# Performance work log

Hardware: AMD Instinct MI355X
Metric: run time of the kernel (lower is better)

## Reference

```python
import jax, jax.numpy as jnp
import numpy as np

HIDDEN_DIM = 2048
HEAD_NUM = 16
HEAD_DIM = HIDDEN_DIM // HEAD_NUM


def setup_inputs() -> dict:
    key = jax.random.key(0)
    ks = jax.random.split(key, 9)
    B, S, H = 2, 2048, HIDDEN_DIM
    scale = 1.0 / np.sqrt(H)
    X = jax.random.normal(ks[0], (B, S, H), dtype=jnp.float32)
    Wq = jax.random.normal(ks[1], (H, H), dtype=jnp.float32) * scale
    bq = jnp.zeros((H,), dtype=jnp.float32)
    Wk = jax.random.normal(ks[2], (H, H), dtype=jnp.float32) * scale
    bk = jnp.zeros((H,), dtype=jnp.float32)
    Wv = jax.random.normal(ks[3], (H, H), dtype=jnp.float32) * scale
    bv = jnp.zeros((H,), dtype=jnp.float32)
    Wo = jax.random.normal(ks[4], (H, H), dtype=jnp.float32) * scale
    bo = jnp.zeros((H,), dtype=jnp.float32)
    return {"X": X, "Wq": Wq, "bq": bq, "Wk": Wk, "bk": bk,
            "Wv": Wv, "bv": bv, "Wo": Wo, "bo": bo}


def reference(X, Wq, bq, Wk, bk, Wv, bv, Wo, bo):
    B, S, H = X.shape
    # QKV projections (nn.Linear applies x @ W.T + b; weights here stored as [in, out])
    Q = X @ Wq + bq
    K = X @ Wk + bk
    V = X @ Wv + bv
    # [B, heads, S, head_dim]
    q = Q.reshape(B, S, HEAD_NUM, HEAD_DIM).transpose(0, 2, 1, 3)
    k = K.reshape(B, S, HEAD_NUM, HEAD_DIM).transpose(0, 2, 1, 3)
    v = V.reshape(B, S, HEAD_NUM, HEAD_DIM).transpose(0, 2, 1, 3)
    scores = jnp.einsum('bhqd,bhkd->bhqk', q, k) / jnp.sqrt(jnp.float32(HEAD_DIM))
    attn = jax.nn.softmax(scores, axis=-1)  # dropout = identity in eval
    out = jnp.einsum('bhqk,bhkd->bhqd', attn, v)
    out = out.transpose(0, 2, 1, 3).reshape(B, S, H)
    return out @ Wo + bo
```

## Files before the change

### kernel.cpp

```cpp
#include <hip/hip_runtime.h>
#include <hip/hip_bf16.h>
#include <stdint.h>


#define Bc 2
#define Sc 2048
#define Hc 2048
#define NHc 16
#define Dc 128
#define Mc 4096

typedef unsigned short ushortT;
typedef float f32x4 __attribute__((ext_vector_type(4)));
typedef _Float16 f16x8 __attribute__((ext_vector_type(8)));

#define MFMAH(a, b, c) __builtin_amdgcn_mfma_f32_16x16x32_f16((a), (b), (c), 0, 0, 0)

static __device__ __forceinline__ ushortT f2h(float x) {
    _Float16 h = (_Float16)x;
    return __builtin_bit_cast(unsigned short, h);
}

static __device__ __forceinline__ void load_lds16(const ushortT* g, ushortT* l) {
    __builtin_amdgcn_global_load_lds(
        (__attribute__((address_space(1))) void*)(g),
        (__attribute__((address_space(3))) void*)(l), 16, 0, 0);
}

__global__ __launch_bounds__(256) void pack_a(
    const float* __restrict__ src, ushortT* __restrict__ dst)
{
    const int mt = blockIdx.x, kt = blockIdx.y;
    const int t = threadIdx.x;
    const int kq = t & 15;
    const int r0 = t >> 4;
    ushortT* tile = dst + ((size_t)(mt * 32 + kt)) * 8192;
#pragma unroll
    for (int rr = 0; rr < 8; ++rr) {
        const int row = r0 + rr * 16;
        const float4 v = *(const float4*)(src + (size_t)(mt * 128 + row) * Hc + kt * 64 + kq * 4);
        _Float16 h[4] = {(_Float16)v.x, (_Float16)v.y, (_Float16)v.z, (_Float16)v.w};
        const int gid = kq >> 1, halfg = kq & 1;
        const int gp = gid ^ (row & 7);
        *(uint2*)(tile + (size_t)row * 64 + gp * 8 + halfg * 4) = *(uint2*)h;
    }
}

__global__ __launch_bounds__(256) void pack_b(
    const float* __restrict__ W0, const float* __restrict__ W1,
    const float* __restrict__ W2, const float* __restrict__ W3,
    ushortT* __restrict__ dst)
{
    const int nt = blockIdx.x, kt = blockIdx.y, which = blockIdx.z;
    const float* W = (which == 0) ? W0 : (which == 1) ? W1 : (which == 2) ? W2 : W3;
    const int t = threadIdx.x;
    const int n = t & 127;
    const int g0 = (t >> 7) * 4;
    ushortT* tile = dst + (size_t)which * 4194304 + ((size_t)(nt * 32 + kt)) * 8192;
#pragma unroll
    for (int gi = 0; gi < 4; ++gi) {
        const int g = g0 + gi;
        _Float16 h[8];
#pragma unroll
        for (int j = 0; j < 8; ++j)
            h[j] = (_Float16)W[(size_t)(kt * 64 + g * 8 + j) * Hc + nt * 128 + n];
        const int gp = g ^ (n & 7);
        *(uint4*)(tile + (size_t)n * 64 + gp * 8) = *(uint4*)h;
    }
}

#define GEMM_PROLOGUE()                                                        \
    __shared__ __align__(16) ushortT As[8192], Bs[8192];                       \
    const int tid = threadIdx.x, wv_ = tid >> 6, lane = tid & 63;              \
    const int lane16 = lane & 15, quad = lane >> 4;                            \
    const int quad4 = quad * 4;                                                \
    const int wm = (wv_ & 1) * 64, wn = (wv_ >> 1) * 64;                       \
    int aoff[4][2], boff[4][2];                                                \
    _Pragma("unroll") for (int mi = 0; mi < 4; ++mi)                           \
        _Pragma("unroll") for (int kf = 0; kf < 2; ++kf) {                     \
            const int ra = wm + mi * 16 + lane16;                              \
            aoff[mi][kf] = ra * 64 + (((kf * 4 + quad) ^ (ra & 7)) << 3);      \
            const int rb = wn + mi * 16 + lane16;                              \
            boff[mi][kf] = rb * 64 + (((kf * 4 + quad) ^ (rb & 7)) << 3);      \
        }                                                                      \
    f32x4 acc[4][4];                                                           \
    _Pragma("unroll") for (int i = 0; i < 4; ++i)                              \
        _Pragma("unroll") for (int j = 0; j < 4; ++j) {                        \
            acc[i][j][0] = 0.f; acc[i][j][1] = 0.f;                            \
            acc[i][j][2] = 0.f; acc[i][j][3] = 0.f; }                          \
    ushortT* asd = &As[wv_ * 2048];                                            \
    ushortT* bsd = &Bs[wv_ * 2048];

#define GEMM_KLOOP(at, bt)                                                     \
    for (int kt2 = 0; kt2 < 32; ++kt2) {                                       \
        _Pragma("unroll") for (int i = 0; i < 4; ++i) {                        \
            load_lds16(at + i * 512 + lane * 8, asd + i * 512);                \
            load_lds16(bt + i * 512 + lane * 8, bsd + i * 512);                \
        }                                                                      \
        at += 8192; bt += 8192;                                                \
        __syncthreads();                                                       \
        _Pragma("unroll") for (int kf = 0; kf < 2; ++kf) {                     \
            f16x8 a[4], b[4];                                                  \
            _Pragma("unroll") for (int mi = 0; mi < 4; ++mi)                   \
                a[mi] = *(const f16x8*)&As[aoff[mi][kf]];                      \
            _Pragma("unroll") for (int nj = 0; nj < 4; ++nj)                   \
                b[nj] = *(const f16x8*)&Bs[boff[nj][kf]];                      \
            _Pragma("unroll") for (int nj = 0; nj < 4; ++nj)                   \
                _Pragma("unroll") for (int mi = 0; mi < 4; ++mi)               \
                    acc[mi][nj] = MFMAH(a[mi], b[nj], acc[mi][nj]);            \
        }                                                                      \
        __syncthreads();                                                       \
    }

__global__ __launch_bounds__(256) void qkv_gemm(
    const ushortT* __restrict__ Xp, const ushortT* __restrict__ Wall,
    const float* __restrict__ bq, const float* __restrict__ bk,
    const float* __restrict__ bv,
    ushortT* __restrict__ Qd, ushortT* __restrict__ Kd, ushortT* __restrict__ Vt)
{
    const int which = blockIdx.x >> 4;
    const int nt = blockIdx.x & 15;
    const int mt = blockIdx.y;
    const ushortT* Wp = Wall + (size_t)which * 4194304;
    const float* bias = (which == 0) ? bq : (which == 1) ? bk : bv;

    GEMM_PROLOGUE();

    const ushortT* at = Xp + (size_t)(mt * 32) * 8192 + wv_ * 2048;
    const ushortT* bt = Wp + (size_t)(nt * 32) * 8192 + wv_ * 2048;
    GEMM_KLOOP(at, bt);

    const float QS = 0.08838834764831845f * 1.4426950408889634f;
#pragma unroll
    for (int nj = 0; nj < 4; ++nj) {
        const int col = nt * 128 + wn + nj * 16 + lane16;
        const float bb = bias[col];
        const int hh = col >> 7, dd = col & 127;
#pragma unroll
        for (int mi = 0; mi < 4; ++mi)
#pragma unroll
            for (int r = 0; r < 4; ++r) {
                const int m = mt * 128 + wm + mi * 16 + quad4 + r;
                const int b = m >> 11, s = m & 2047;
                float v = acc[mi][nj][r] + bb;
                if (which == 0)
                    Qd[(((size_t)(b * NHc + hh)) * Sc + s) * Dc + dd] = f2h(v * QS);
                else if (which == 1)
                    Kd[(((size_t)(b * NHc + hh)) * Sc + s) * Dc + dd] = f2h(v);
                else
                    Vt[(((size_t)(b * NHc + hh)) * Dc + dd) * Sc + s] = f2h(v);
            }
    }
}

__global__ __launch_bounds__(256) void attn(
    const ushortT* __restrict__ Qd, const ushortT* __restrict__ Kd,
    const ushortT* __restrict__ Vt, ushortT* __restrict__ AOp)
{
    const int qt = blockIdx.x, hh = blockIdx.y, bb = blockIdx.z;
    const ushortT* Qp = Qd + ((size_t)(bb * NHc + hh)) * Sc * Dc;
    const ushortT* Kp = Kd + ((size_t)(bb * NHc + hh)) * Sc * Dc;
    const ushortT* Vp = Vt + ((size_t)(bb * NHc + hh)) * Dc * Sc;

    __shared__ __align__(16) ushortT Ks[64 * 128];
    __shared__ __align__(16) ushortT Vs[128 * 64];
    __shared__ __align__(16) float   SsF[4 * 32 * 64];
    __shared__ float alphas[4 * 32], linvs[4 * 32];

    const int tid = threadIdx.x, wv_ = tid >> 6, lane = tid & 63;
    const int lane16 = lane & 15, quad = lane >> 4;
    const int quad8 = quad * 8, quad4 = quad * 4;
    const int s0 = qt * 128 + wv_ * 32;

    f16x8 q[2][4];
#pragma unroll
    for (int mi = 0; mi < 2; ++mi)
#pragma unroll
        for (int kf = 0; kf < 4; ++kf)
            q[mi][kf] = *(const f16x8*)(Qp + (size_t)(s0 + mi * 16 + lane16) * Dc + kf * 32 + quad8);

    f32x4 o[2][8];
#pragma unroll
    for (int mi = 0; mi < 2; ++mi)
#pragma unroll
        for (int dj = 0; dj < 8; ++dj) { o[mi][dj][0] = 0.f; o[mi][dj][1] = 0.f; o[mi][dj][2] = 0.f; o[mi][dj][3] = 0.f; }

    float m_run = -1e30f, l_run = 0.f;
    const int sr = lane >> 1, sch = (lane & 1) * 32;
    const int kr = tid >> 2, kseg = tid & 3;
    const int vr = tid >> 1, vseg = tid & 1;
    float* Sw = &SsF[wv_ * 2048];
    ushortT* Pw = (ushortT*)Sw;

    for (int nt = 0; nt < 32; ++nt) {
        const ushortT* ksrc = Kp + (size_t)(nt * 64 + kr) * Dc + kseg * 32;
#pragma unroll
        for (int i = 0; i < 4; ++i)
            *(uint4*)&Ks[kr * 128 + (((kseg * 4 + i) ^ (kr & 7)) << 3)] = *(const uint4*)(ksrc + i * 8);
        const ushortT* vsrc = Vp + (size_t)vr * Sc + nt * 64 + vseg * 32;
#pragma unroll
        for (int i = 0; i < 4; ++i)
            *(uint4*)&Vs[vr * 64 + (((vseg * 4 + i) ^ (vr & 7)) << 3)] = *(const uint4*)(vsrc + i * 8);
        __syncthreads();

        f32x4 sacc[2][4];
#pragma unroll
        for (int mi = 0; mi < 2; ++mi)
#pragma unroll
            for (int nj = 0; nj < 4; ++nj) { sacc[mi][nj][0] = 0.f; sacc[mi][nj][1] = 0.f; sacc[mi][nj][2] = 0.f; sacc[mi][nj][3] = 0.f; }
#pragma unroll
        for (int kf = 0; kf < 4; ++kf) {
            f16x8 kb[4];
#pragma unroll
            for (int nj = 0; nj < 4; ++nj) {
                const int row = nj * 16 + lane16;
                kb[nj] = *(const f16x8*)&Ks[row * 128 + (((kf * 4 + quad) ^ (row & 7)) << 3)];
            }
#pragma unroll
            for (int mi = 0; mi < 2; ++mi)
#pragma unroll
                for (int nj = 0; nj < 4; ++nj)
                    sacc[mi][nj] = MFMAH(q[mi][kf], kb[nj], sacc[mi][nj]);
        }
#pragma unroll
        for (int mi = 0; mi < 2; ++mi)
#pragma unroll
            for (int nj = 0; nj < 4; ++nj)
#pragma unroll
                for (int r = 0; r < 4; ++r) {
                    const int row = mi * 16 + quad4 + r, col = nj * 16 + lane16;
                    Sw[row * 64 + (((col >> 2) ^ (row & 15)) << 2) + (col & 3)] = sacc[mi][nj][r];
                }
        float svv[32];
#pragma unroll
        for (int i = 0; i < 8; ++i)
            *(float4*)&svv[i * 4] = *(const float4*)&Sw[sr * 64 + ((((sch >> 2) + i) ^ (sr & 15)) << 2)];
        float mx = svv[0];
#pragma unroll
        for (int i = 1; i < 32; ++i) mx = fmaxf(mx, svv[i]);
        mx = fmaxf(mx, __shfl_xor(mx, 1));
        const float mnew = fmaxf(m_run, mx);
        const float alpha = exp2f(m_run - mnew);
        m_run = mnew;
        float sum = 0.f;
#pragma unroll
        for (int i = 0; i < 32; ++i) { const float p = exp2f(svv[i] - mnew); svv[i] = p; sum += p; }
        sum += __shfl_xor(sum, 1);
        l_run = l_run * alpha + sum;
        if (!(lane & 1)) alphas[wv_ * 32 + sr] = alpha;
        uint32_t pu[16];
#pragma unroll
        for (int i = 0; i < 16; ++i)
            pu[i] = (uint32_t)f2h(svv[2 * i]) | ((uint32_t)f2h(svv[2 * i + 1]) << 16);
#pragma unroll
        for (int i = 0; i < 4; ++i)
            *(uint4*)&Pw[sr * 64 + ((((sch >> 3) + i) ^ (sr & 7)) << 3)] = *(uint4*)&pu[i * 4];
#pragma unroll
        for (int mi = 0; mi < 2; ++mi)
#pragma unroll
            for (int r = 0; r < 4; ++r) {
                const int row = mi * 16 + quad4 + r;
                const float av = alphas[wv_ * 32 + row];
#pragma unroll
                for (int dj = 0; dj < 8; ++dj) o[mi][dj][r] *= av;
            }
#pragma unroll
        for (int kf2 = 0; kf2 < 2; ++kf2) {
            f16x8 pa[2];
#pragma unroll
            for (int mi = 0; mi < 2; ++mi) {
                const int row = mi * 16 + lane16;
                pa[mi] = *(const f16x8*)&Pw[row * 64 + (((kf2 * 4 + quad) ^ (row & 7)) << 3)];
            }
#pragma unroll
            for (int dj = 0; dj < 8; ++dj) {
                const int row = dj * 16 + lane16;
                const f16x8 vb = *(const f16x8*)&Vs[row * 64 + (((kf2 * 4 + quad) ^ (row & 7)) << 3)];
#pragma unroll
                for (int mi = 0; mi < 2; ++mi)
                    o[mi][dj] = MFMAH(pa[mi], vb, o[mi][dj]);
            }
        }
        __syncthreads();
    }

    if (!(lane & 1)) linvs[wv_ * 32 + sr] = 1.f / l_run;
#pragma unroll
    for (int mi = 0; mi < 2; ++mi)
#pragma unroll
        for (int r = 0; r < 4; ++r) {
            const int row = mi * 16 + quad4 + r;
            const float li = linvs[wv_ * 32 + row];
            const int mrow = bb * Sc + qt * 128 + wv_ * 32 + row;
            const int mtile = mrow >> 7, rin = mrow & 127;
#pragma unroll
            for (int dj = 0; dj < 8; ++dj) {
                const int kt = hh * 2 + (dj >> 2);
                const int colin = (dj & 3) * 16 + lane16;
                const int g = colin >> 3, e = colin & 7;
                const int gp = g ^ (rin & 7);
                AOp[((size_t)(mtile * 32 + kt)) * 8192 + rin * 64 + gp * 8 + e] =
                    f2h(o[mi][dj][r] * li);
            }
        }
}

__global__ __launch_bounds__(256) void out_gemm(
    const ushortT* __restrict__ AOp, const ushortT* __restrict__ Wop,
    const float* __restrict__ bo, float* __restrict__ out)
{
    const int nt = blockIdx.x;
    const int mt = blockIdx.y;

    GEMM_PROLOGUE();

    const ushortT* at = AOp + (size_t)(mt * 32) * 8192 + wv_ * 2048;
    const ushortT* bt = Wop + (size_t)(nt * 32) * 8192 + wv_ * 2048;
    GEMM_KLOOP(at, bt);

#pragma unroll
    for (int nj = 0; nj < 4; ++nj) {
        const int col = nt * 128 + wn + nj * 16 + lane16;
        const float bb = bo[col];
#pragma unroll
        for (int mi = 0; mi < 4; ++mi)
#pragma unroll
            for (int r = 0; r < 4; ++r) {
                const int m = mt * 128 + wm + mi * 16 + quad4 + r;
                out[(size_t)m * Hc + col] = acc[mi][nj][r] + bb;
            }
    }
}

extern "C" void kernel_launch(void* const* d_in, const int* in_sizes, int n_in,
                              void* d_out, int out_size, void* d_ws, size_t ws_size,
                              hipStream_t stream) {
    (void)in_sizes; (void)n_in; (void)out_size; (void)ws_size;

    const float* X  = (const float*)d_in[0];
    const float* Wq = (const float*)d_in[1];
    const float* bq = (const float*)d_in[2];
    const float* Wk = (const float*)d_in[3];
    const float* bk = (const float*)d_in[4];
    const float* Wv = (const float*)d_in[5];
    const float* bv = (const float*)d_in[6];
    const float* Wo = (const float*)d_in[7];
    const float* bo = (const float*)d_in[8];
    float* out = (float*)d_out;

    ushortT* ws = (ushortT*)d_ws;
    const size_t E = (size_t)Mc * Hc;
    const size_t WE = (size_t)Hc * Hc;
    ushortT* Xp   = ws;
    ushortT* Wall = Xp + E;
    ushortT* Qd   = Wall + 4 * WE;
    ushortT* Kd   = Qd + E;
    ushortT* Vt   = Kd + E;
    ushortT* AOp  = Vt + E;

    pack_a<<<dim3(32, 32), 256, 0, stream>>>(X, Xp);
    pack_b<<<dim3(16, 32, 4), 256, 0, stream>>>(Wq, Wk, Wv, Wo, Wall);
    qkv_gemm<<<dim3(48, 32), 256, 0, stream>>>(Xp, Wall, bq, bk, bv, Qd, Kd, Vt);
    attn<<<dim3(16, NHc, Bc), 256, 0, stream>>>(Qd, Kd, Vt, AOp);
    out_gemm<<<dim3(16, 32), 256, 0, stream>>>(AOp, Wall + 3 * WE, bo, out);
}
```

Baseline: 523.0 us.

## Pre-tile K/V in LDS layout, use direct global-to-LDS loads, shrink softmax scratch

The QKV GEMM epilogue now writes K and V tiles already swizzled in the 64-row LDS layout, so the attention kernel can copy them with global_load_lds instead of register round trips. Softmax is processed per 16-row half using a smaller padded score buffer and separate P buffer, cutting LDS use to allow two blocks per CU (launch_bounds 256,2). V fragments are hoisted into registers once per tile. The cost is scattered epilogue stores and higher register pressure from the hoisted V fragments.

```diff
diff --git a/kernel.cpp b/kernel.cpp
--- a/kernel.cpp
+++ b/kernel.cpp
@@ -142,30 +142,39 @@
             for (int r = 0; r < 4; ++r) {
                 const int m = mt * 128 + wm + mi * 16 + quad4 + r;
                 const int b = m >> 11, s = m & 2047;
-                float v = acc[mi][nj][r] + bb;
-                if (which == 0)
-                    Qd[(((size_t)(b * NHc + hh)) * Sc + s) * Dc + dd] = f2h(v * QS);
-                else if (which == 1)
-                    Kd[(((size_t)(b * NHc + hh)) * Sc + s) * Dc + dd] = f2h(v);
-                else
-                    Vt[(((size_t)(b * NHc + hh)) * Dc + dd) * Sc + s] = f2h(v);
-            }
-    }
-}
-
-__global__ __launch_bounds__(256) void attn(
-    const ushortT* __restrict__ Qd, const ushortT* __restrict__ Kd,
+                const float v = acc[mi][nj][r] + bb;
+                const size_t bhb = (size_t)(b * NHc + hh) * (Sc * Dc);
+                if (which == 0) {
+                    Qd[bhb + (size_t)s * Dc + dd] = f2h(v * QS);
+                } else if (which == 1) {
+                    const int t2 = s >> 6, sin = s & 63;
+                    Kd[bhb + (size_t)t2 * 8192 + sin * 128 +
+                       (((dd >> 3) ^ (sin & 7)) << 3) + (dd & 7)] = f2h(v);
+                } else {
+                    const int t2 = s >> 6, sin = s & 63;
+                    Vt[bhb + (size_t)t2 * 8192 + dd * 64 +
+                       (((sin >> 3) ^ (dd & 7)) << 3) + (sin & 7)] = f2h(v);
+                }
+            }
+    }
+}
+
+#define SSTR 68
+
+__global__ __launch_bounds__(256, 2) void attn(
+    const ushortT* __restrict__ Qd, const ushortT* __restrict__ Kt,
     const ushortT* __restrict__ Vt, ushortT* __restrict__ AOp)
 {
     const int qt = blockIdx.x, hh = blockIdx.y, bb = blockIdx.z;
-    const ushortT* Qp = Qd + ((size_t)(bb * NHc + hh)) * Sc * Dc;
-    const ushortT* Kp = Kd + ((size_t)(bb * NHc + hh)) * Sc * Dc;
-    const ushortT* Vp = Vt + ((size_t)(bb * NHc + hh)) * Dc * Sc;
-
-    __shared__ __align__(16) ushortT Ks[64 * 128];
-    __shared__ __align__(16) ushortT Vs[128 * 64];
-    __shared__ __align__(16) float   SsF[4 * 32 * 64];
-    __shared__ float alphas[4 * 32], linvs[4 * 32];
+    const ushortT* Qp  = Qd + ((size_t)(bb * NHc + hh)) * Sc * Dc;
+    const ushortT* Kbh = Kt + ((size_t)(bb * NHc + hh)) * Sc * Dc;
+    const ushortT* Vbh = Vt + ((size_t)(bb * NHc + hh)) * Sc * Dc;
+
+    __shared__ __align__(16) ushortT Ks[8192];
+    __shared__ __align__(16) ushortT Vs[8192];
+    __shared__ __align__(16) float   Sbuf[4][16 * SSTR];
+    __shared__ __align__(16) ushortT Pbuf[4][1024];
+    __shared__ float alphas[4][32], linvs[4][32];
 
     const int tid = threadIdx.x, wv_ = tid >> 6, lane = tid & 63;
     const int lane16 = lane & 15, quad = lane >> 4;
@@ -185,22 +194,22 @@
 #pragma unroll
         for (int dj = 0; dj < 8; ++dj) { o[mi][dj][0] = 0.f; o[mi][dj][1] = 0.f; o[mi][dj][2] = 0.f; o[mi][dj][3] = 0.f; }
 
-    float m_run = -1e30f, l_run = 0.f;
-    const int sr = lane >> 1, sch = (lane & 1) * 32;
-    const int kr = tid >> 2, kseg = tid & 3;
-    const int vr = tid >> 1, vseg = tid & 1;
-    float* Sw = &SsF[wv_ * 2048];
-    ushortT* Pw = (ushortT*)Sw;
+    float m_run[2] = {-1e30f, -1e30f}, l_run[2] = {0.f, 0.f};
+    const int srow = lane >> 2;
+    const int scol = (lane & 3) * 16;
+    float*   Sw = Sbuf[wv_];
+    ushortT* Pw = Pbuf[wv_];
 
     for (int nt = 0; nt < 32; ++nt) {
-        const ushortT* ksrc = Kp + (size_t)(nt * 64 + kr) * Dc + kseg * 32;
-#pragma unroll
-        for (int i = 0; i < 4; ++i)
-            *(uint4*)&Ks[kr * 128 + (((kseg * 4 + i) ^ (kr & 7)) << 3)] = *(const uint4*)(ksrc + i * 8);
-        const ushortT* vsrc = Vp + (size_t)vr * Sc + nt * 64 + vseg * 32;
-#pragma unroll
-        for (int i = 0; i < 4; ++i)
-            *(uint4*)&Vs[vr * 64 + (((vseg * 4 + i) ^ (vr & 7)) << 3)] = *(const uint4*)(vsrc + i * 8);
+        const ushortT* ktile = Kbh + (size_t)nt * 8192 + wv_ * 2048;
+        const ushortT* vtile = Vbh + (size_t)nt * 8192 + wv_ * 2048;
+        ushortT* kdst = Ks + wv_ * 2048;
+        ushortT* vdst = Vs + wv_ * 2048;
+#pragma unroll
+        for (int i = 0; i < 4; ++i) {
+            load_lds16(ktile + i * 512 + lane * 8, kdst + i * 512);
+            load_lds16(vtile + i * 512 + lane * 8, vdst + i * 512);
+        }
         __syncthreads();
 
         f32x4 sacc[2][4];
@@ -222,84 +231,87 @@
                 for (int nj = 0; nj < 4; ++nj)
                     sacc[mi][nj] = MFMAH(q[mi][kf], kb[nj], sacc[mi][nj]);
         }
-#pragma unroll
-        for (int mi = 0; mi < 2; ++mi)
-#pragma unroll
-            for (int nj = 0; nj < 4; ++nj)
-#pragma unroll
-                for (int r = 0; r < 4; ++r) {
-                    const int row = mi * 16 + quad4 + r, col = nj * 16 + lane16;
-                    Sw[row * 64 + (((col >> 2) ^ (row & 15)) << 2) + (col & 3)] = sacc[mi][nj][r];
-                }
-        float svv[32];
-#pragma unroll
-        for (int i = 0; i < 8; ++i)
-            *(float4*)&svv[i * 4] = *(const float4*)&Sw[sr * 64 + ((((sch >> 2) + i) ^ (sr & 15)) << 2)];
-        float mx = svv[0];
-#pragma unroll
-        for (int i = 1; i < 32; ++i) mx = fmaxf(mx, svv[i]);
-        mx = fmaxf(mx, __shfl_xor(mx, 1));
-        const float mnew = fmaxf(m_run, mx);
-        const float alpha = exp2f(m_run - mnew);
-        m_run = mnew;
-        float sum = 0.f;
-#pragma unroll
-        for (int i = 0; i < 32; ++i) { const float p = exp2f(svv[i] - mnew); svv[i] = p; sum += p; }
-        sum += __shfl_xor(sum, 1);
-        l_run = l_run * alpha + sum;
-        if (!(lane & 1)) alphas[wv_ * 32 + sr] = alpha;
-        uint32_t pu[16];
-#pragma unroll
-        for (int i = 0; i < 16; ++i)
-            pu[i] = (uint32_t)f2h(svv[2 * i]) | ((uint32_t)f2h(svv[2 * i + 1]) << 16);
-#pragma unroll
-        for (int i = 0; i < 4; ++i)
-            *(uint4*)&Pw[sr * 64 + ((((sch >> 3) + i) ^ (sr & 7)) << 3)] = *(uint4*)&pu[i * 4];
-#pragma unroll
-        for (int mi = 0; mi < 2; ++mi)
-#pragma unroll
-            for (int r = 0; r < 4; ++r) {
-                const int row = mi * 16 + quad4 + r;
-                const float av = alphas[wv_ * 32 + row];
-#pragma unroll
-                for (int dj = 0; dj < 8; ++dj) o[mi][dj][r] *= av;
-            }
-#pragma unroll
-        for (int kf2 = 0; kf2 < 2; ++kf2) {
-            f16x8 pa[2];
-#pragma unroll
-            for (int mi = 0; mi < 2; ++mi) {
-                const int row = mi * 16 + lane16;
-                pa[mi] = *(const f16x8*)&Pw[row * 64 + (((kf2 * 4 + quad) ^ (row & 7)) << 3)];
-            }
+
+        f16x8 vb[2][8];
+#pragma unroll
+        for (int kf2 = 0; kf2 < 2; ++kf2)
 #pragma unroll
             for (int dj = 0; dj < 8; ++dj) {
                 const int row = dj * 16 + lane16;
-                const f16x8 vb = *(const f16x8*)&Vs[row * 64 + (((kf2 * 4 + quad) ^ (row & 7)) << 3)];
-#pragma unroll
-                for (int mi = 0; mi < 2; ++mi)
-                    o[mi][dj] = MFMAH(pa[mi], vb, o[mi][dj]);
+                vb[kf2][dj] = *(const f16x8*)&Vs[row * 64 + (((kf2 * 4 + quad) ^ (row & 7)) << 3)];
+            }
+
+#pragma unroll
+        for (int mi = 0; mi < 2; ++mi) {
+#pragma unroll
+            for (int nj = 0; nj < 4; ++nj)
+#pragma unroll
+                for (int r = 0; r < 4; ++r)
+                    Sw[(quad4 + r) * SSTR + nj * 16 + lane16] = sacc[mi][nj][r];
+            float sv[16];
+#pragma unroll
+            for (int i = 0; i < 4; ++i)
+                *(float4*)&sv[i * 4] = *(const float4*)&Sw[srow * SSTR + scol + i * 4];
+            float mx = sv[0];
+#pragma unroll
+            for (int i = 1; i < 16; ++i) mx = fmaxf(mx, sv[i]);
+            mx = fmaxf(mx, __shfl_xor(mx, 1));
+            mx = fmaxf(mx, __shfl_xor(mx, 2));
+            const float mnew = fmaxf(m_run[mi], mx);
+            const float alpha = exp2f(m_run[mi] - mnew);
+            m_run[mi] = mnew;
+            float sum = 0.f;
+#pragma unroll
+            for (int i = 0; i < 16; ++i) { const float p = exp2f(sv[i] - mnew); sv[i] = p; sum += p; }
+            sum += __shfl_xor(sum, 1);
+            sum += __shfl_xor(sum, 2);
+            l_run[mi] = l_run[mi] * alpha + sum;
+            if ((lane & 3) == 0) alphas[wv_][mi * 16 + srow] = alpha;
+            uint32_t pu[8];
+#pragma unroll
+            for (int i = 0; i < 8; ++i)
+                pu[i] = (uint32_t)f2h(sv[2 * i]) | ((uint32_t)f2h(sv[2 * i + 1]) << 16);
+#pragma unroll
+            for (int j = 0; j < 2; ++j) {
+                const int g = (scol >> 3) + j;
+                *(uint4*)&Pw[srow * 64 + ((g ^ (srow & 7)) << 3)] = *(uint4*)&pu[j * 4];
+            }
+#pragma unroll
+            for (int r = 0; r < 4; ++r) {
+                const float av = alphas[wv_][mi * 16 + quad4 + r];
+#pragma unroll
+                for (int dj = 0; dj < 8; ++dj) o[mi][dj][r] *= av;
+            }
+#pragma unroll
+            for (int kf2 = 0; kf2 < 2; ++kf2) {
+                const f16x8 pa = *(const f16x8*)&Pw[lane16 * 64 + (((kf2 * 4 + quad) ^ (lane16 & 7)) << 3)];
+#pragma unroll
+                for (int dj = 0; dj < 8; ++dj)
+                    o[mi][dj] = MFMAH(pa, vb[kf2][dj], o[mi][dj]);
             }
         }
         __syncthreads();
     }
 
-    if (!(lane & 1)) linvs[wv_ * 32 + sr] = 1.f / l_run;
+    if ((lane & 3) == 0) {
+        linvs[wv_][srow]      = 1.f / l_run[0];
+        linvs[wv_][16 + srow] = 1.f / l_run[1];
+    }
 #pragma unroll
     for (int mi = 0; mi < 2; ++mi)
 #pragma unroll
         for (int r = 0; r < 4; ++r) {
             const int row = mi * 16 + quad4 + r;
-            const float li = linvs[wv_ * 32 + row];
+            const float li = linvs[wv_][row];
             const int mrow = bb * Sc + qt * 128 + wv_ * 32 + row;
             const int mtile = mrow >> 7, rin = mrow & 127;
 #pragma unroll
             for (int dj = 0; dj < 8; ++dj) {
-                const int kt = hh * 2 + (dj >> 2);
+                const int kt2 = hh * 2 + (dj >> 2);
                 const int colin = (dj & 3) * 16 + lane16;
                 const int g = colin >> 3, e = colin & 7;
                 const int gp = g ^ (rin & 7);
-                AOp[((size_t)(mtile * 32 + kt)) * 8192 + rin * 64 + gp * 8 + e] =
+                AOp[((size_t)(mtile * 32 + kt2)) * 8192 + rin * 64 + gp * 8 + e] =
                     f2h(o[mi][dj][r] * li);
             }
         }
@@ -355,12 +367,12 @@
     ushortT* Wall = Xp + E;
     ushortT* Qd   = Wall + 4 * WE;
     ushortT* Kd   = Qd + E;
-    ushortT* Vt   = Kd + E;
-    ushortT* AOp  = Vt + E;
+    ushortT* Vtp  = Kd + E;
+    ushortT* AOp  = Vtp + E;
 
     pack_a<<<dim3(32, 32), 256, 0, stream>>>(X, Xp);
     pack_b<<<dim3(16, 32, 4), 256, 0, stream>>>(Wq, Wk, Wv, Wo, Wall);
-    qkv_gemm<<<dim3(48, 32), 256, 0, stream>>>(Xp, Wall, bq, bk, bv, Qd, Kd, Vt);
-    attn<<<dim3(16, NHc, Bc), 256, 0, stream>>>(Qd, Kd, Vt, AOp);
+    qkv_gemm<<<dim3(48, 32), 256, 0, stream>>>(Xp, Wall, bq, bk, bv, Qd, Kd, Vtp);
+    attn<<<dim3(16, NHc, Bc), 256, 0, stream>>>(Qd, Kd, Vtp, AOp);
     out_gemm<<<dim3(16, 32), 256, 0, stream>>>(AOp, Wall + 3 * WE, bo, out);
 }
```

After: 452.9 us. -13.4%, faster.
